# Kernel optimization log

Measured on AMD Instinct MI355X. Metric: run time of the kernel, lower is better.

Reference implementation:

```python
import jax, jax.numpy as jnp
import numpy as np

N = 100000
E = 3200000


def setup_inputs() -> dict:
    key = jax.random.key(0)
    ks = jax.random.split(key, 12)
    x = jax.random.normal(ks[0], (N, 124), dtype=jnp.float32)
    pos = jax.random.normal(ks[1], (N, 3), dtype=jnp.float32)
    z = jax.random.normal(ks[2], (N,), dtype=jnp.float32)
    edge_index = jax.random.randint(ks[3], (2, E), 0, N, dtype=jnp.int64)
    def lin(k, fin, fout):
        kw, kb = jax.random.split(k)
        s = 1.0 / np.sqrt(fin)
        W = jax.random.uniform(kw, (fin, fout), minval=-s, maxval=s, dtype=jnp.float32)
        b = jax.random.uniform(kb, (fout,), minval=-s, maxval=s, dtype=jnp.float32)
        return W, b
    W1, b1 = lin(ks[4], 128, 256)
    W2, b2 = lin(ks[5], 256, 256)
    W3, b3 = lin(ks[6], 256, 256)
    W4, b4 = lin(ks[7], 256, 1)
    return {"x": x, "pos": pos, "z": z, "edge_index": edge_index,
            "W1": W1, "b1": b1, "W2": W2, "b2": b2,
            "W3": W3, "b3": b3, "W4": W4, "b4": b4}


def reference(x, pos, z, edge_index, W1, b1, W2, b2, W3, b3, W4, b4):
    # features = hstack(x, pos, z[:, None])  -> [N, input_dim]
    feats = jnp.concatenate([x, pos, z[:, None]], axis=1)
    src, dst = edge_index[0], edge_index[1]
    # sum of neighbor (dst) features into each src node: O(E) segment-sum
    sums = jax.ops.segment_sum(feats[dst], src, num_segments=feats.shape[0])
    # per-node L2 normalize (matches torch.linalg.norm per row)
    h = sums / jnp.linalg.norm(sums, axis=1, keepdims=True)
    h = jax.nn.relu(h @ W1 + b1)
    h = jax.nn.relu(h @ W2 + b2)
    h = jax.nn.relu(h @ W3 + b3)
    h = h @ W4 + b4            # [N, 1]
    return jnp.mean(h, axis=0)  # [1]
```

## Files before the change

### kernel.cpp

```cpp
#include <hip/hip_runtime.h>
#include <math.h>

#define N_NODES 100000
#define N_EDGES 3200000
#define BSHIFT 6
#define NBUCK 1563
#define NBLK_E 256
#define EPB 12500
#define CAP 3072

typedef _Float16 half8 __attribute__((ext_vector_type(8)));
typedef float f32x4 __attribute__((ext_vector_type(4)));
typedef float f32x2 __attribute__((ext_vector_type(2)));

__device__ __forceinline__ void gload16(const void* gsrc, void* ldst) {
    __builtin_amdgcn_global_load_lds(
        (const __attribute__((address_space(1))) unsigned int*)gsrc,
        (__attribute__((address_space(3))) unsigned int*)ldst,
        16, 0, 0);
}

__global__ __launch_bounds__(256) void pack_kernel(
    const float* __restrict__ x, const float* __restrict__ pos,
    const float* __restrict__ z, unsigned int* __restrict__ feats8)
{
    int idx = blockIdx.x * blockDim.x + threadIdx.x;
    if (idx >= N_NODES * 32) return;
    int n = idx >> 5, j = idx & 31;
    float v[4];
    #pragma unroll
    for (int k = 0; k < 4; ++k) {
        int f = j * 4 + k;
        if (f < 124)      v[k] = x[n * 124 + f];
        else if (f < 127) v[k] = pos[n * 3 + (f - 124)];
        else              v[k] = z[n];
    }
    int u = 0;
    u = __builtin_amdgcn_cvt_pk_fp8_f32(v[0], v[1], u, false);
    u = __builtin_amdgcn_cvt_pk_fp8_f32(v[2], v[3], u, true);
    feats8[idx] = (unsigned int)u;
}

__global__ __launch_bounds__(256) void wprep_kernel(
    const float* __restrict__ W, int K, _Float16* __restrict__ WT)
{
    int idx = blockIdx.x * blockDim.x + threadIdx.x;
    if (idx >= K * 256) return;
    int k = idx >> 8, c = idx & 255;
    WT[c * K + k] = (_Float16)W[idx];
}

__global__ __launch_bounds__(1024) void coarse_hist_kernel(
    const int* __restrict__ ei, int* __restrict__ gcnt)
{
    __shared__ int bins[NBUCK];
    int t = threadIdx.x, blk = blockIdx.x;
    for (int b = t; b < NBUCK; b += 1024) bins[b] = 0;
    __syncthreads();
    int base = blk * EPB;
    for (int i = t; i < EPB; i += 1024) {
        int src = __builtin_nontemporal_load(&ei[base + i]);
        atomicAdd(&bins[src >> BSHIFT], 1);
    }
    __syncthreads();
    for (int b = t; b < NBUCK; b += 1024)
        gcnt[blk * NBUCK + b] = bins[b];
}

__global__ __launch_bounds__(256) void bucket_tot_kernel(
    const int* __restrict__ gcnt, int* __restrict__ btot)
{
    __shared__ int red[4];
    int b = blockIdx.x, t = threadIdx.x;
    int s = gcnt[t * NBUCK + b];
    #pragma unroll
    for (int off = 32; off > 0; off >>= 1) s += __shfl_xor(s, off, 64);
    if ((t & 63) == 0) red[t >> 6] = s;
    __syncthreads();
    if (t == 0) btot[b] = red[0] + red[1] + red[2] + red[3];
}

__global__ __launch_bounds__(1024) void scan_buckets_kernel(
    const int* __restrict__ btot, int* __restrict__ bbase)
{
    __shared__ int s[1024];
    int t = threadIdx.x;
    int i0 = 2 * t, i1 = 2 * t + 1;
    int v0 = (i0 < NBUCK) ? btot[i0] : 0;
    int v1 = (i1 < NBUCK) ? btot[i1] : 0;
    int sum = v0 + v1;
    s[t] = sum;
    __syncthreads();
    for (int off = 1; off < 1024; off <<= 1) {
        int o = (t >= off) ? s[t - off] : 0;
        __syncthreads();
        s[t] += o;
        __syncthreads();
    }
    int excl = s[t] - sum;
    if (i0 < NBUCK) bbase[i0] = excl;
    if (i1 < NBUCK) bbase[i1] = excl + v0;
    if (i0 == NBUCK - 1) bbase[NBUCK] = excl + v0;
    if (i1 == NBUCK - 1) bbase[NBUCK] = excl + v0 + v1;
}

__global__ __launch_bounds__(256) void colscan_kernel(
    const int* __restrict__ gcnt, const int* __restrict__ bbase,
    int* __restrict__ gbase)
{
    __shared__ int s[NBLK_E];
    int b = blockIdx.x, t = threadIdx.x;
    int v = gcnt[t * NBUCK + b];
    s[t] = v;
    __syncthreads();
    for (int off = 1; off < NBLK_E; off <<= 1) {
        int o = (t >= off) ? s[t - off] : 0;
        __syncthreads();
        s[t] += o;
        __syncthreads();
    }
    gbase[t * NBUCK + b] = bbase[b] + s[t] - v;
}

__global__ __launch_bounds__(1024) void bucket_scatter_kernel(
    const int* __restrict__ ei, const int* __restrict__ gcnt,
    const int* __restrict__ gbase, unsigned int* __restrict__ bucketed)
{
    __shared__ unsigned int val[EPB];
    __shared__ int gd[EPB];
    __shared__ int cur[NBUCK];
    __shared__ int gofs[NBUCK];
    __shared__ int ssum[1024];

    int t = threadIdx.x, blk = blockIdx.x;

    int i0 = 2 * t, i1 = 2 * t + 1;
    int c0 = (i0 < NBUCK) ? gcnt[blk * NBUCK + i0] : 0;
    int c1 = (i1 < NBUCK) ? gcnt[blk * NBUCK + i1] : 0;
    int sum = c0 + c1;
    ssum[t] = sum;
    __syncthreads();
    for (int off = 1; off < 1024; off <<= 1) {
        int o = (t >= off) ? ssum[t - off] : 0;
        __syncthreads();
        ssum[t] += o;
        __syncthreads();
    }
    int excl = ssum[t] - sum;
    if (i0 < NBUCK) { cur[i0] = excl;      gofs[i0] = gbase[blk * NBUCK + i0] - excl; }
    if (i1 < NBUCK) { cur[i1] = excl + c0; gofs[i1] = gbase[blk * NBUCK + i1] - (excl + c0); }
    __syncthreads();

    int base = blk * EPB;
    for (int i = t; i < EPB; i += 1024) {
        int e = base + i;
        int src = __builtin_nontemporal_load(&ei[e]);
        int dst = __builtin_nontemporal_load(&ei[N_EDGES + e]);
        int b = src >> BSHIFT;
        int r = atomicAdd(&cur[b], 1);
        val[r] = (unsigned int)dst | ((unsigned int)(src & 63) << 17);
        gd[r] = gofs[b] + r;
    }
    __syncthreads();

    for (int i = t; i < EPB; i += 1024)
        bucketed[gd[i]] = val[i];
}

__global__ __launch_bounds__(256) void sortagg_kernel(
    const int* __restrict__ bbase, const unsigned int* __restrict__ bucketed,
    const unsigned int* __restrict__ feats8, _Float16* __restrict__ h0)
{
    __shared__ unsigned int srt[CAP];
    __shared__ int excl[64], cur[64];

    int t = threadIdx.x, b = blockIdx.x;
    int segs = bbase[b], cnt = bbase[b + 1] - segs;
    if (cnt > CAP) cnt = CAP;

    if (t < 64) cur[t] = 0;
    __syncthreads();

    for (int i = t; i < cnt; i += 256)
        atomicAdd(&cur[(bucketed[segs + i] >> 17) & 63], 1);
    __syncthreads();

    int v = (t < 64) ? cur[t] : 0;
    if (t < 64) excl[t] = v;
    __syncthreads();
    for (int off = 1; off < 64; off <<= 1) {
        int o = (t >= off && t < 64) ? excl[t - off] : 0;
        __syncthreads();
        if (t < 64) excl[t] += o;
        __syncthreads();
    }
    if (t < 64) { excl[t] -= v; cur[t] = excl[t]; }
    __syncthreads();

    for (int i = t; i < cnt; i += 256) {
        unsigned int p = bucketed[segs + i];
        int r = atomicAdd(&cur[(p >> 17) & 63], 1);
        if (r < CAP) srt[r] = p & 0x1FFFFu;
    }
    __syncthreads();

    int w = t >> 6, lane = t & 63;
    int h = lane >> 5, s = lane & 31;
    const unsigned int* fb = feats8 + s;
    f32x2 p;

#define ACC4(U)                                                     \
    p = __builtin_amdgcn_cvt_pk_f32_fp8((U), false);                \
    a0 += p[0]; a1 += p[1];                                         \
    p = __builtin_amdgcn_cvt_pk_f32_fp8((U), true);                 \
    a2 += p[0]; a3 += p[1];

    for (int j = 0; j < 16; ++j) {
        int nl = w * 16 + j;
        int node = b * 64 + nl;
        if (node >= N_NODES) break;
        int start = excl[nl], end = cur[nl];
        float a0 = 0.f, a1 = 0.f, a2 = 0.f, a3 = 0.f;
        int i = start;
        for (; i + 16 <= end; i += 16) {
            int d0 = srt[i + h];
            int d1 = srt[i + 2 + h];
            int d2 = srt[i + 4 + h];
            int d3 = srt[i + 6 + h];
            int d4 = srt[i + 8 + h];
            int d5 = srt[i + 10 + h];
            int d6 = srt[i + 12 + h];
            int d7 = srt[i + 14 + h];
            unsigned int u0 = fb[(long long)d0 * 32];
            unsigned int u1 = fb[(long long)d1 * 32];
            unsigned int u2 = fb[(long long)d2 * 32];
            unsigned int u3 = fb[(long long)d3 * 32];
            unsigned int u4 = fb[(long long)d4 * 32];
            unsigned int u5 = fb[(long long)d5 * 32];
            unsigned int u6 = fb[(long long)d6 * 32];
            unsigned int u7 = fb[(long long)d7 * 32];
            ACC4(u0); ACC4(u1); ACC4(u2); ACC4(u3);
            ACC4(u4); ACC4(u5); ACC4(u6); ACC4(u7);
        }
        for (; i + 2 <= end; i += 2) {
            unsigned int u = fb[(long long)srt[i + h] * 32];
            ACC4(u);
        }
        if (i < end && h == 0) {
            unsigned int u = fb[(long long)srt[i] * 32];
            ACC4(u);
        }
        a0 += __shfl_xor(a0, 32, 64);
        a1 += __shfl_xor(a1, 32, 64);
        a2 += __shfl_xor(a2, 32, 64);
        a3 += __shfl_xor(a3, 32, 64);
        float ss = a0 * a0 + a1 * a1 + a2 * a2 + a3 * a3;
        #pragma unroll
        for (int off = 16; off > 0; off >>= 1) ss += __shfl_xor(ss, off, 64);
        float inv = 1.0f / sqrtf(ss);
        if (h == 0) {
            union { uint2 u; _Float16 f[4]; } o;
            o.f[0] = (_Float16)(a0 * inv); o.f[1] = (_Float16)(a1 * inv);
            o.f[2] = (_Float16)(a2 * inv); o.f[3] = (_Float16)(a3 * inv);
            *reinterpret_cast<uint2*>(&h0[(long long)node * 128 + s * 4]) = o.u;
        }
    }
#undef ACC4
}

__global__ __launch_bounds__(256, 2) void fused_mlp_kernel(
    const _Float16* __restrict__ h0,
    const _Float16* __restrict__ WT1,
    const float* __restrict__ b1,
    const _Float16* __restrict__ WT2,
    const float* __restrict__ b2,
    const _Float16* __restrict__ WT3,
    const float* __restrict__ b3,
    const float* __restrict__ W4,
    float* __restrict__ partials, int M)
{
    __shared__ __align__(16) _Float16 sA[8 * 2048];
    __shared__ __align__(16) _Float16 sB[2][256 * 32];
    __shared__ float redf[4];

    const int t = threadIdx.x;
    const int row0 = blockIdx.x * 64;

    const int ar = t >> 2, ap = t & 3;
    const int ag = ap ^ ((ar >> 1) & 3);
    int arow = row0 + ar; if (arow > M - 1) arow = M - 1;
    const _Float16* aSrc = h0 + (long long)arow * 128 + ag * 8;

    const int bc0 = t >> 2;
    const int gb = ap ^ ((bc0 >> 1) & 3);

    const int w = t >> 6, lane = t & 63;
    const int wr = w >> 1, wc = w & 1;
    const int lrow = lane & 15, g = lane >> 4;

    unsigned int offA[2], offB[8];
    #pragma unroll
    for (int rt = 0; rt < 2; ++rt) {
        int r = wr * 32 + rt * 16 + lrow;
        offA[rt] = r * 64 + (g ^ ((r >> 1) & 3)) * 16;
    }
    #pragma unroll
    for (int ct = 0; ct < 8; ++ct) {
        int cidx = wc * 128 + ct * 16 + lrow;
        offB[ct] = cidx * 64 + (g ^ ((cidx >> 1) & 3)) * 16;
    }

    f32x4 acc[2][8];
    #pragma unroll
    for (int i = 0; i < 2; ++i)
        #pragma unroll
        for (int j = 0; j < 8; ++j)
            acc[i][j] = (f32x4){0.f, 0.f, 0.f, 0.f};

#define STAGE_B(WT, Kv, KC, BUF)                                             \
    {                                                                        \
        _Pragma("unroll")                                                    \
        for (int j = 0; j < 4; ++j)                                          \
            gload16((WT) + (long long)(bc0 + j * 64) * (Kv) + gb * 8 +       \
                        (KC) * 32,                                           \
                    (char*)(BUF) + j * 4096 + t * 16);                       \
    }

#define STORE_ACTS(BIAS)                                                     \
    {                                                                        \
        _Pragma("unroll")                                                    \
        for (int ct = 0; ct < 8; ++ct) {                                     \
            int col = wc * 128 + ct * 16 + lrow;                             \
            float bb = (BIAS)[col];                                          \
            int chk = col >> 5, kk = col & 31;                               \
            int kg = kk >> 3, ke = kk & 7;                                   \
            _Pragma("unroll")                                                \
            for (int rt = 0; rt < 2; ++rt) {                                 \
                _Pragma("unroll")                                            \
                for (int jj = 0; jj < 4; ++jj) {                             \
                    int rowl = wr * 32 + rt * 16 + g * 4 + jj;               \
                    int slot = kg ^ ((rowl >> 1) & 3);                       \
                    sA[chk * 2048 + rowl * 32 + slot * 8 + ke] =             \
                        (_Float16)fmaxf(acc[rt][ct][jj] + bb, 0.f);          \
                    acc[rt][ct][jj] = 0.f;                                   \
                }                                                            \
            }                                                                \
        }                                                                    \
    }

#define MFMA_CHUNK(KC, BUF)                                                  \
    {                                                                        \
        half8 a[2], b[8];                                                    \
        _Pragma("unroll")                                                    \
        for (int rt = 0; rt < 2; ++rt)                                       \
            a[rt] = *reinterpret_cast<const half8*>(                         \
                (const char*)sA + (KC) * 4096 + offA[rt]);                   \
        _Pragma("unroll")                                                    \
        for (int ct = 0; ct < 8; ++ct)                                       \
            b[ct] = *reinterpret_cast<const half8*>(                         \
                (const char*)(BUF) + offB[ct]);                              \
        _Pragma("unroll")                                                    \
        for (int rt = 0; rt < 2; ++rt)                                       \
            _Pragma("unroll")                                                \
            for (int ct = 0; ct < 8; ++ct)                                   \
                acc[rt][ct] = __builtin_amdgcn_mfma_f32_16x16x32_f16(        \
                    a[rt], b[ct], acc[rt][ct], 0, 0, 0);                     \
    }

    #pragma unroll
    for (int kc = 0; kc < 4; ++kc)
        gload16(aSrc + kc * 32, (char*)sA + kc * 4096 + t * 16);
    STAGE_B(WT1, 128, 0, sB[0]);
    __syncthreads();

    int cur = 0;

    #pragma unroll
    for (int kc = 0; kc < 4; ++kc) {
        if (kc < 3) { STAGE_B(WT1, 128, kc + 1, sB[cur ^ 1]); }
        else        { STAGE_B(WT2, 256, 0,      sB[cur ^ 1]); }
        MFMA_CHUNK(kc, sB[cur]);
        __syncthreads();
        cur ^= 1;
    }
    STORE_ACTS(b1);
    __syncthreads();

    #pragma unroll
    for (int kc = 0; kc < 8; ++kc) {
        if (kc < 7) { STAGE_B(WT2, 256, kc + 1, sB[cur ^ 1]); }
        else        { STAGE_B(WT3, 256, 0,      sB[cur ^ 1]); }
        MFMA_CHUNK(kc, sB[cur]);
        __syncthreads();
        cur ^= 1;
    }
    STORE_ACTS(b2);
    __syncthreads();

    #pragma unroll
    for (int kc = 0; kc < 8; ++kc) {
        if (kc < 7) { STAGE_B(WT3, 256, kc + 1, sB[cur ^ 1]); }
        MFMA_CHUNK(kc, sB[cur]);
        __syncthreads();
        cur ^= 1;
    }

    float sum = 0.f;
    #pragma unroll
    for (int ct = 0; ct < 8; ++ct) {
        int col = wc * 128 + ct * 16 + lrow;
        float bb = b3[col];
        float w4 = W4[col];
        #pragma unroll
        for (int rt = 0; rt < 2; ++rt) {
            #pragma unroll
            for (int jj = 0; jj < 4; ++jj) {
                int row = row0 + wr * 32 + rt * 16 + g * 4 + jj;
                if (row < M) {
                    float v = fmaxf(acc[rt][ct][jj] + bb, 0.f);
                    sum += v * w4;
                }
            }
        }
    }
    #pragma unroll
    for (int off = 32; off > 0; off >>= 1) sum += __shfl_xor(sum, off, 64);
    if (lane == 0) redf[w] = sum;
    __syncthreads();
    if (t == 0) partials[blockIdx.x] = redf[0] + redf[1] + redf[2] + redf[3];
#undef STAGE_B
#undef STORE_ACTS
#undef MFMA_CHUNK
}

__global__ __launch_bounds__(256) void final_kernel(
    const float* __restrict__ partials, int n,
    const float* __restrict__ b4, float* __restrict__ out)
{
    __shared__ float buf[256];
    float s = 0.f;
    for (int i = threadIdx.x; i < n; i += 256) s += partials[i];
    buf[threadIdx.x] = s;
    __syncthreads();
    for (int off = 128; off > 0; off >>= 1) {
        if (threadIdx.x < off) buf[threadIdx.x] += buf[threadIdx.x + off];
        __syncthreads();
    }
    if (threadIdx.x == 0) out[0] = buf[0] / (float)N_NODES + b4[0];
}

extern "C" void kernel_launch(void* const* d_in, const int* in_sizes, int n_in,
                              void* d_out, int out_size, void* d_ws, size_t ws_size,
                              hipStream_t stream)
{
    const float* x   = (const float*)d_in[0];
    const float* pos = (const float*)d_in[1];
    const float* z   = (const float*)d_in[2];
    const int*   ei  = (const int*)d_in[3];
    const float* W1  = (const float*)d_in[4];
    const float* b1  = (const float*)d_in[5];
    const float* W2  = (const float*)d_in[6];
    const float* b2  = (const float*)d_in[7];
    const float* W3  = (const float*)d_in[8];
    const float* b3  = (const float*)d_in[9];
    const float* W4  = (const float*)d_in[10];
    const float* b4  = (const float*)d_in[11];
    float* out = (float*)d_out;

    char* ws = (char*)d_ws;
    unsigned int* feats8   = (unsigned int*)(ws);
    _Float16*     h0       = (_Float16*)    (ws + 12800000);
    int*          gcnt     = (int*)         (ws + 38400000);
    int*          gbase    = (int*)         (ws + 40000512);
    int*          btot     = (int*)         (ws + 41601024);
    int*          bbase    = (int*)         (ws + 41607276);
    unsigned int* bucketed = (unsigned int*)(ws + 41613532);
    _Float16*     WT1      = (_Float16*)    (ws + 54413568);
    _Float16*     WT2      = (_Float16*)    (ws + 54479104);
    _Float16*     WT3      = (_Float16*)    (ws + 54610176);
    float*        partials = (float*)       (ws + 54741248);

    const int gblocks = (N_NODES + 63) / 64;

    wprep_kernel<<<(128 * 256 + 255) / 256, 256, 0, stream>>>(W1, 128, WT1);
    wprep_kernel<<<(256 * 256 + 255) / 256, 256, 0, stream>>>(W2, 256, WT2);
    wprep_kernel<<<(256 * 256 + 255) / 256, 256, 0, stream>>>(W3, 256, WT3);

    pack_kernel<<<(N_NODES * 32 + 255) / 256, 256, 0, stream>>>(x, pos, z, feats8);

    coarse_hist_kernel<<<NBLK_E, 1024, 0, stream>>>(ei, gcnt);
    bucket_tot_kernel<<<NBUCK, 256, 0, stream>>>(gcnt, btot);
    scan_buckets_kernel<<<1, 1024, 0, stream>>>(btot, bbase);
    colscan_kernel<<<NBUCK, 256, 0, stream>>>(gcnt, bbase, gbase);
    bucket_scatter_kernel<<<NBLK_E, 1024, 0, stream>>>(ei, gcnt, gbase, bucketed);

    sortagg_kernel<<<NBUCK, 256, 0, stream>>>(bbase, bucketed, feats8, h0);

    fused_mlp_kernel<<<gblocks, 256, 0, stream>>>(
        h0, WT1, b1, WT2, b2, WT3, b3, W4, partials, N_NODES);

    final_kernel<<<1, 256, 0, stream>>>(partials, gblocks, b4, out);
}
```

Before: 191.6 us.

## Triple-buffer MLP weight staging with manual waitcnt barriers; widen gather unroll

The fused MLP kernel moves from a double-buffered to a triple-buffered B-tile pipeline. Weight loads are issued two stages ahead, and explicit vmcnt waits with raw s_barrier replace __syncthreads, plus setprio around the MFMA blocks and biases hoisted into registers. The aggregation kernel's gather loop is widened to 24 edges per iteration and accumulates in packed f32x2 registers. This aims to hide global-to-LDS weight load latency and raise memory-level parallelism in the gather, at the cost of more LDS and more registers, which may lower occupancy.

New measurement: 179.2 us. 6.5% less time.

```diff
diff --git a/kernel.cpp b/kernel.cpp
--- a/kernel.cpp
+++ b/kernel.cpp
@@ -207,40 +207,33 @@
     int w = t >> 6, lane = t & 63;
     int h = lane >> 5, s = lane & 31;
     const unsigned int* fb = feats8 + s;
-    f32x2 p;
 
 #define ACC4(U)                                                     \
-    p = __builtin_amdgcn_cvt_pk_f32_fp8((U), false);                \
-    a0 += p[0]; a1 += p[1];                                         \
-    p = __builtin_amdgcn_cvt_pk_f32_fp8((U), true);                 \
-    a2 += p[0]; a3 += p[1];
+    a01 += __builtin_amdgcn_cvt_pk_f32_fp8((U), false);             \
+    a23 += __builtin_amdgcn_cvt_pk_f32_fp8((U), true);
 
     for (int j = 0; j < 16; ++j) {
         int nl = w * 16 + j;
         int node = b * 64 + nl;
         if (node >= N_NODES) break;
         int start = excl[nl], end = cur[nl];
-        float a0 = 0.f, a1 = 0.f, a2 = 0.f, a3 = 0.f;
+        f32x2 a01 = {0.f, 0.f}, a23 = {0.f, 0.f};
         int i = start;
-        for (; i + 16 <= end; i += 16) {
-            int d0 = srt[i + h];
-            int d1 = srt[i + 2 + h];
-            int d2 = srt[i + 4 + h];
-            int d3 = srt[i + 6 + h];
-            int d4 = srt[i + 8 + h];
-            int d5 = srt[i + 10 + h];
-            int d6 = srt[i + 12 + h];
-            int d7 = srt[i + 14 + h];
-            unsigned int u0 = fb[(long long)d0 * 32];
-            unsigned int u1 = fb[(long long)d1 * 32];
-            unsigned int u2 = fb[(long long)d2 * 32];
-            unsigned int u3 = fb[(long long)d3 * 32];
-            unsigned int u4 = fb[(long long)d4 * 32];
-            unsigned int u5 = fb[(long long)d5 * 32];
-            unsigned int u6 = fb[(long long)d6 * 32];
-            unsigned int u7 = fb[(long long)d7 * 32];
-            ACC4(u0); ACC4(u1); ACC4(u2); ACC4(u3);
-            ACC4(u4); ACC4(u5); ACC4(u6); ACC4(u7);
+        for (; i + 24 <= end; i += 24) {
+            unsigned int uu[12];
+            #pragma unroll
+            for (int q = 0; q < 12; ++q)
+                uu[q] = fb[(long long)srt[i + 2 * q + h] * 32];
+            #pragma unroll
+            for (int q = 0; q < 12; ++q) { ACC4(uu[q]); }
+        }
+        for (; i + 8 <= end; i += 8) {
+            unsigned int uu[4];
+            #pragma unroll
+            for (int q = 0; q < 4; ++q)
+                uu[q] = fb[(long long)srt[i + 2 * q + h] * 32];
+            #pragma unroll
+            for (int q = 0; q < 4; ++q) { ACC4(uu[q]); }
         }
         for (; i + 2 <= end; i += 2) {
             unsigned int u = fb[(long long)srt[i + h] * 32];
@@ -250,6 +243,7 @@
             unsigned int u = fb[(long long)srt[i] * 32];
             ACC4(u);
         }
+        float a0 = a01[0], a1 = a01[1], a2 = a23[0], a3 = a23[1];
         a0 += __shfl_xor(a0, 32, 64);
         a1 += __shfl_xor(a1, 32, 64);
         a2 += __shfl_xor(a2, 32, 64);
@@ -280,8 +274,7 @@
     float* __restrict__ partials, int M)
 {
     __shared__ __align__(16) _Float16 sA[8 * 2048];
-    __shared__ __align__(16) _Float16 sB[2][256 * 32];
-    __shared__ float redf[4];
+    __shared__ __align__(16) _Float16 sB[3][8192];
 
     const int t = threadIdx.x;
     const int row0 = blockIdx.x * 64;
@@ -310,6 +303,14 @@
         offB[ct] = cidx * 64 + (g ^ ((cidx >> 1) & 3)) * 16;
     }
 
+    float bb1[8], bb2[8], bb3[8], w4v[8];
+    #pragma unroll
+    for (int ct = 0; ct < 8; ++ct) {
+        int col = wc * 128 + ct * 16 + lrow;
+        bb1[ct] = b1[col]; bb2[ct] = b2[col];
+        bb3[ct] = b3[col]; w4v[ct] = W4[col];
+    }
+
     f32x4 acc[2][8];
     #pragma unroll
     for (int i = 0; i < 2; ++i)
@@ -317,21 +318,33 @@
         for (int j = 0; j < 8; ++j)
             acc[i][j] = (f32x4){0.f, 0.f, 0.f, 0.f};
 
-#define STAGE_B(WT, Kv, KC, BUF)                                             \
+#define STG(WT, Kv, KC, BUF)                                                 \
     {                                                                        \
         _Pragma("unroll")                                                    \
         for (int j = 0; j < 4; ++j)                                          \
             gload16((WT) + (long long)(bc0 + j * 64) * (Kv) + gb * 8 +       \
                         (KC) * 32,                                           \
-                    (char*)(BUF) + j * 4096 + t * 16);                       \
-    }
-
-#define STORE_ACTS(BIAS)                                                     \
+                    (char*)sB[BUF] + j * 4096 + t * 16);                     \
+    }
+
+#define WB(N)                                                                \
+    asm volatile("s_waitcnt vmcnt(" #N ")" ::: "memory");                    \
+    __builtin_amdgcn_s_barrier();                                            \
+    __builtin_amdgcn_sched_barrier(0);
+
+#define EB() __builtin_amdgcn_s_barrier();
+
+#define SEAM()                                                               \
+    asm volatile("s_waitcnt lgkmcnt(0)" ::: "memory");                       \
+    __builtin_amdgcn_s_barrier();                                            \
+    __builtin_amdgcn_sched_barrier(0);
+
+#define STORE_ACTS(BB)                                                       \
     {                                                                        \
         _Pragma("unroll")                                                    \
         for (int ct = 0; ct < 8; ++ct) {                                     \
             int col = wc * 128 + ct * 16 + lrow;                             \
-            float bb = (BIAS)[col];                                          \
+            float bb = (BB)[ct];                                             \
             int chk = col >> 5, kk = col & 31;                               \
             int kg = kk >> 3, ke = kk & 7;                                   \
             _Pragma("unroll")                                                \
@@ -350,85 +363,80 @@
 
 #define MFMA_CHUNK(KC, BUF)                                                  \
     {                                                                        \
-        half8 a[2], b[8];                                                    \
+        half8 a[2], bfr[8];                                                  \
+        __builtin_amdgcn_s_setprio(1);                                       \
         _Pragma("unroll")                                                    \
         for (int rt = 0; rt < 2; ++rt)                                       \
             a[rt] = *reinterpret_cast<const half8*>(                         \
                 (const char*)sA + (KC) * 4096 + offA[rt]);                   \
         _Pragma("unroll")                                                    \
         for (int ct = 0; ct < 8; ++ct)                                       \
-            b[ct] = *reinterpret_cast<const half8*>(                         \
-                (const char*)(BUF) + offB[ct]);                              \
+            bfr[ct] = *reinterpret_cast<const half8*>(                       \
+                (const char*)sB[BUF] + offB[ct]);                            \
         _Pragma("unroll")                                                    \
         for (int rt = 0; rt < 2; ++rt)                                       \
             _Pragma("unroll")                                                \
             for (int ct = 0; ct < 8; ++ct)                                   \
                 acc[rt][ct] = __builtin_amdgcn_mfma_f32_16x16x32_f16(        \
-                    a[rt], b[ct], acc[rt][ct], 0, 0, 0);                     \
+                    a[rt], bfr[ct], acc[rt][ct], 0, 0, 0);                   \
+        __builtin_amdgcn_s_setprio(0);                                       \
     }
 
     #pragma unroll
     for (int kc = 0; kc < 4; ++kc)
         gload16(aSrc + kc * 32, (char*)sA + kc * 4096 + t * 16);
-    STAGE_B(WT1, 128, 0, sB[0]);
-    __syncthreads();
-
-    int cur = 0;
-
-    #pragma unroll
-    for (int kc = 0; kc < 4; ++kc) {
-        if (kc < 3) { STAGE_B(WT1, 128, kc + 1, sB[cur ^ 1]); }
-        else        { STAGE_B(WT2, 256, 0,      sB[cur ^ 1]); }
-        MFMA_CHUNK(kc, sB[cur]);
-        __syncthreads();
-        cur ^= 1;
-    }
-    STORE_ACTS(b1);
-    __syncthreads();
-
-    #pragma unroll
-    for (int kc = 0; kc < 8; ++kc) {
-        if (kc < 7) { STAGE_B(WT2, 256, kc + 1, sB[cur ^ 1]); }
-        else        { STAGE_B(WT3, 256, 0,      sB[cur ^ 1]); }
-        MFMA_CHUNK(kc, sB[cur]);
-        __syncthreads();
-        cur ^= 1;
-    }
-    STORE_ACTS(b2);
-    __syncthreads();
-
-    #pragma unroll
-    for (int kc = 0; kc < 8; ++kc) {
-        if (kc < 7) { STAGE_B(WT3, 256, kc + 1, sB[cur ^ 1]); }
-        MFMA_CHUNK(kc, sB[cur]);
-        __syncthreads();
-        cur ^= 1;
-    }
+    STG(WT1, 128, 0, 0) STG(WT1, 128, 1, 1)
+
+    STG(WT1, 128, 2, 2)  WB(8)  MFMA_CHUNK(0, 0)  EB()
+    STG(WT1, 128, 3, 0)  WB(8)  MFMA_CHUNK(1, 1)  EB()
+    STG(WT2, 256, 0, 1)  WB(8)  MFMA_CHUNK(2, 2)  EB()
+    STG(WT2, 256, 1, 2)  WB(8)  MFMA_CHUNK(3, 0)  EB()
+    STORE_ACTS(bb1) SEAM()
+    STG(WT2, 256, 2, 0)  WB(8)  MFMA_CHUNK(0, 1)  EB()
+    STG(WT2, 256, 3, 1)  WB(8)  MFMA_CHUNK(1, 2)  EB()
+    STG(WT2, 256, 4, 2)  WB(8)  MFMA_CHUNK(2, 0)  EB()
+    STG(WT2, 256, 5, 0)  WB(8)  MFMA_CHUNK(3, 1)  EB()
+    STG(WT2, 256, 6, 1)  WB(8)  MFMA_CHUNK(4, 2)  EB()
+    STG(WT2, 256, 7, 2)  WB(8)  MFMA_CHUNK(5, 0)  EB()
+    STG(WT3, 256, 0, 0)  WB(8)  MFMA_CHUNK(6, 1)  EB()
+    STG(WT3, 256, 1, 1)  WB(8)  MFMA_CHUNK(7, 2)  EB()
+    STORE_ACTS(bb2) SEAM()
+    STG(WT3, 256, 2, 2)  WB(8)  MFMA_CHUNK(0, 0)  EB()
+    STG(WT3, 256, 3, 0)  WB(8)  MFMA_CHUNK(1, 1)  EB()
+    STG(WT3, 256, 4, 1)  WB(8)  MFMA_CHUNK(2, 2)  EB()
+    STG(WT3, 256, 5, 2)  WB(8)  MFMA_CHUNK(3, 0)  EB()
+    STG(WT3, 256, 6, 0)  WB(8)  MFMA_CHUNK(4, 1)  EB()
+    STG(WT3, 256, 7, 1)  WB(8)  MFMA_CHUNK(5, 2)  EB()
+                         WB(4)  MFMA_CHUNK(6, 0)  EB()
+                         WB(0)  MFMA_CHUNK(7, 1)  EB()
 
     float sum = 0.f;
     #pragma unroll
     for (int ct = 0; ct < 8; ++ct) {
-        int col = wc * 128 + ct * 16 + lrow;
-        float bb = b3[col];
-        float w4 = W4[col];
+        float bb = bb3[ct];
+        float w4 = w4v[ct];
         #pragma unroll
         for (int rt = 0; rt < 2; ++rt) {
             #pragma unroll
             for (int jj = 0; jj < 4; ++jj) {
                 int row = row0 + wr * 32 + rt * 16 + g * 4 + jj;
                 if (row < M) {
-                    float v = fmaxf(acc[rt][ct][jj] + bb, 0.f);
-                    sum += v * w4;
+                    float vv = fmaxf(acc[rt][ct][jj] + bb, 0.f);
+                    sum += vv * w4;
                 }
             }
         }
     }
     #pragma unroll
     for (int off = 32; off > 0; off >>= 1) sum += __shfl_xor(sum, off, 64);
+    float* redf = reinterpret_cast<float*>(sA);
     if (lane == 0) redf[w] = sum;
     __syncthreads();
     if (t == 0) partials[blockIdx.x] = redf[0] + redf[1] + redf[2] + redf[3];
-#undef STAGE_B
+#undef STG
+#undef WB
+#undef EB
+#undef SEAM
 #undef STORE_ACTS
 #undef MFMA_CHUNK
 }
```
